# Optimization experiments

Hardware: AMD Instinct MI355X
Metric: run time of the kernel (lower is better)

Reference implementation:

```python
import jax, jax.numpy as jnp
import numpy as np

B, N, C = 8, 1024, 768
H = 12
HD = C // H  # 64
SCALE = HD ** -0.5


def setup_inputs() -> dict:
    key = jax.random.key(0)
    k1, k2, k3, k4 = jax.random.split(key, 4)
    x = jax.random.normal(k1, (B, N, C), dtype=jnp.float32)
    # torch Linear weights are [out, in]; qkv has no bias (qkv_bias=False)
    w_qkv = jax.random.normal(k2, (3 * C, C), dtype=jnp.float32) * (C ** -0.5)
    w_proj = jax.random.normal(k3, (C, C), dtype=jnp.float32) * (C ** -0.5)
    b_proj = jax.random.normal(k4, (C,), dtype=jnp.float32) * 0.01
    return {"x": x, "w_qkv": w_qkv, "w_proj": w_proj, "b_proj": b_proj}


def reference(x, w_qkv, w_proj, b_proj):
    b, n, c = x.shape
    # qkv: [B, N, 3C] -> [3, B, H, N, HD]
    qkv = (x @ w_qkv.T).reshape(b, n, 3, H, c // H).transpose(2, 0, 3, 1, 4)
    q, k, v = qkv[0], qkv[1], qkv[2]
    attn = jnp.einsum('bhqd,bhkd->bhqk', q, k) * SCALE
    attn = jax.nn.softmax(attn, axis=-1)
    out = jnp.einsum('bhqk,bhkd->bhqd', attn, v)          # [B, H, N, HD]
    out = out.transpose(0, 2, 1, 3).reshape(b, n, c)      # [B, N, C]
    out = out @ w_proj.T + b_proj
    return out
```

## Files before the change

kernel.cpp:

```cpp
#include <hip/hip_runtime.h>
#include <hip/hip_bf16.h>
#include <cstdint>

#define TB 8
#define TN 1024
#define TC 768
#define TH 12
#define THD 64
#define TM (TB*TN)
#define TNQKV (3*TC)
#define QSCALE_LOG2E 0.18033688011112042f

typedef __attribute__((ext_vector_type(8))) short s16x8;
typedef __attribute__((ext_vector_type(4))) float f32x4;
typedef __attribute__((ext_vector_type(16))) float f32x16;
typedef __attribute__((ext_vector_type(2))) unsigned int u32x2;

__device__ __forceinline__ unsigned short f2bf(float f) {
    union { float f; unsigned int u; } v; v.f = f;
    unsigned int u = v.u;
    return (unsigned short)((u + 0x7FFFu + ((u >> 16) & 1u)) >> 16);
}

__device__ __forceinline__ float bf2f(unsigned short h) {
    union { float f; unsigned int u; } v; v.u = ((unsigned int)h) << 16;
    return v.f;
}

__device__ __forceinline__ unsigned int cvt_pk_bf16(float lo, float hi) {
    unsigned int r;
    asm("v_cvt_pk_bf16_f32 %0, %1, %2" : "=v"(r) : "v"(lo), "v"(hi));
    return r;
}

__device__ __forceinline__ void gload_lds16(const unsigned short* g, unsigned short* l) {
    __builtin_amdgcn_global_load_lds(
        (const __attribute__((address_space(1))) unsigned int*)g,
        (__attribute__((address_space(3))) unsigned int*)l,
        16, 0, 0);
}

__global__ __launch_bounds__(256) void cvt3_kernel(
    const float* __restrict__ a, unsigned short* __restrict__ oa, int na,
    const float* __restrict__ b, unsigned short* __restrict__ ob, int nb,
    const float* __restrict__ c, unsigned short* __restrict__ oc, int nc)
{
    int i = blockIdx.x * blockDim.x + threadIdx.x;
    const float* src; unsigned short* dst; int idx;
    if (i < na)           { src = a; dst = oa; idx = i; }
    else if (i < na + nb) { src = b; dst = ob; idx = i - na; }
    else if (i < na + nb + nc) { src = c; dst = oc; idx = i - na - nb; }
    else return;
    f32x4 x0 = *(const f32x4*)(src + (size_t)idx * 8);
    f32x4 x1 = *(const f32x4*)(src + (size_t)idx * 8 + 4);
    s16x8 r;
    #pragma unroll
    for (int e = 0; e < 4; e++) r[e] = (short)f2bf(x0[e]);
    #pragma unroll
    for (int e = 0; e < 4; e++) r[4 + e] = (short)f2bf(x1[e]);
    *(s16x8*)(dst + (size_t)idx * 8) = r;
}

template<bool BIAS, bool OBF16, bool VSPLIT>
__global__ __launch_bounds__(256) void gemm_bt(
    const unsigned short* __restrict__ A,
    const unsigned short* __restrict__ Bm,
    void* __restrict__ Cout,
    const float* __restrict__ bias,
    unsigned short* __restrict__ vt,
    int M, int Nn, int K)
{
    __shared__ unsigned short As[128 * 64];
    __shared__ unsigned short Bs[128 * 64];
    const int t = threadIdx.x;
    const int w = t >> 6, l = t & 63;
    const int wm = w >> 1, wn = w & 1;
    const int bm = blockIdx.x, bn = blockIdx.y;
    const int l31 = l & 31, khi = l >> 5;
    const int r7 = l31 & 7;

    f32x16 acc00 = {}, acc01 = {}, acc10 = {}, acc11 = {};

    const unsigned short* Ab = A + (size_t)bm * 128 * K;
    const unsigned short* Bb = Bm + (size_t)bn * 128 * K;

    for (int kt = 0; kt < K; kt += 64) {
        __syncthreads();
        #pragma unroll
        for (int j = 0; j < 4; j++) {
            const int s = j * 256 + t, row = s >> 3, c = s & 7;
            const int g = c ^ (row & 7);
            gload_lds16(Ab + (size_t)row * K + kt + g * 8, As + s * 8);
            gload_lds16(Bb + (size_t)row * K + kt + g * 8, Bs + s * 8);
        }
        __syncthreads();
        #pragma unroll
        for (int ks = 0; ks < 4; ks++) {
            const int ch = ((ks << 1) + khi) ^ r7;
            const unsigned short* Ar = As + (wm * 64 + l31) * 64 + ch * 8;
            const unsigned short* Br = Bs + (wn * 64 + l31) * 64 + ch * 8;
            s16x8 a0 = *(const s16x8*)(Ar);
            s16x8 a1 = *(const s16x8*)(Ar + 32 * 64);
            s16x8 b0 = *(const s16x8*)(Br);
            s16x8 b1 = *(const s16x8*)(Br + 32 * 64);
            acc00 = __builtin_amdgcn_mfma_f32_32x32x16_bf16(a0, b0, acc00, 0, 0, 0);
            acc01 = __builtin_amdgcn_mfma_f32_32x32x16_bf16(a0, b1, acc01, 0, 0, 0);
            acc10 = __builtin_amdgcn_mfma_f32_32x32x16_bf16(a1, b0, acc10, 0, 0, 0);
            acc11 = __builtin_amdgcn_mfma_f32_32x32x16_bf16(a1, b1, acc11, 0, 0, 0);
        }
    }

    const int r0 = bm * 128 + wm * 64;
    const int c0 = bn * 128 + wn * 64;
    f32x16 accs[2][2] = {{acc00, acc01}, {acc10, acc11}};
    if constexpr (VSPLIT) {
        if (bn >= 12) {
            const int bb = (r0 >> 10) * TH;
            #pragma unroll
            for (int X = 0; X < 2; X++)
                #pragma unroll
                for (int Y = 0; Y < 2; Y++) {
                    const int dg = c0 + Y * 32 + l31 - 2 * TC;
                    unsigned short* vp = vt + ((size_t)(bb + (dg >> 6)) << 16)
                                            + (dg & 63) * TN;
                    const int k0 = (r0 & 1023) + X * 32 + 4 * khi;
                    #pragma unroll
                    for (int g = 0; g < 4; g++) {
                        u32x2 r;
                        r[0] = cvt_pk_bf16(accs[X][Y][g * 4], accs[X][Y][g * 4 + 1]);
                        r[1] = cvt_pk_bf16(accs[X][Y][g * 4 + 2], accs[X][Y][g * 4 + 3]);
                        *(u32x2*)(vp + k0 + 8 * g) = r;
                    }
                }
            return;
        }
    }
    if constexpr (OBF16) {
        unsigned short* O = (unsigned short*)Cout;
        #pragma unroll
        for (int X = 0; X < 2; X++)
            #pragma unroll
            for (int Y = 0; Y < 2; Y++) {
                const int cc = c0 + Y * 32 + l31;
                const int rb = r0 + X * 32 + 4 * khi;
                #pragma unroll
                for (int i = 0; i < 16; i++)
                    O[(size_t)(rb + (i & 3) + 8 * (i >> 2)) * Nn + cc] =
                        f2bf(accs[X][Y][i]);
            }
    } else {
        float* O = (float*)Cout;
        #pragma unroll
        for (int X = 0; X < 2; X++)
            #pragma unroll
            for (int Y = 0; Y < 2; Y++) {
                const int cc = c0 + Y * 32 + l31;
                const int rb = r0 + X * 32 + 4 * khi;
                float bv = 0.f;
                if constexpr (BIAS) bv = bias[cc];
                #pragma unroll
                for (int i = 0; i < 16; i++)
                    O[(size_t)(rb + (i & 3) + 8 * (i >> 2)) * Nn + cc] =
                        accs[X][Y][i] + bv;
            }
    }
}

__global__ __launch_bounds__(512) void attn_kernel(
    const unsigned short* __restrict__ qkv,
    const unsigned short* __restrict__ vt,
    unsigned short* __restrict__ out)
{
    const int bid = blockIdx.x;
    const int vid = (bid & 7) * 96 + (bid >> 3);
    const int bh = vid >> 3;
    const int qt = vid & 7;
    const int b = bh / TH, h = bh % TH;
    const int t = threadIdx.x, w = t >> 6, l = t & 63;
    const int lr = l & 15, lh = l >> 4;
    const int qbase = qt * 128 + w * 16;

    __shared__ unsigned short Kbuf[2][64 * 64];
    __shared__ unsigned short Vbuf[2][64 * 64];
    __shared__ unsigned short plds[8][16 * 64];

    const unsigned short* kbase = qkv + (size_t)(b * TN) * TNQKV + TC + h * THD;
    const unsigned short* vtb = vt + (size_t)bh * THD * TN;

    const int srow_lo = (l >> 3);
    const int schunk = (l & 7) ^ srow_lo;
    const int srow = w * 8 + srow_lo;
    const int sdst = w * 512 + l * 8;

    const unsigned short* qptr = qkv + (size_t)(b * TN + qbase + lr) * TNQKV + h * THD;
    s16x8 bq[2];
    #pragma unroll
    for (int cj = 0; cj < 2; cj++) {
        s16x8 raw = *(const s16x8*)(qptr + cj * 32 + lh * 8);
        #pragma unroll
        for (int e = 0; e < 8; e++)
            bq[cj][e] = (short)f2bf(bf2f((unsigned short)raw[e]) * QSCALE_LOG2E);
    }
    s16x8 av1;
    #pragma unroll
    for (int e = 0; e < 8; e++) av1[e] = (short)0x3F80;

    f32x4 o[5] = {};
    unsigned short* pw = plds[w];
    const int lr7 = lr & 7;

    gload_lds16(kbase + (size_t)srow * TNQKV + schunk * 8, &Kbuf[0][sdst]);
    gload_lds16(vtb + (size_t)srow * TN + schunk * 8, &Vbuf[0][sdst]);
    __syncthreads();

    for (int it = 0; it < 16; it++) {
        const int kt = it * 64;
        const int cur = it & 1, nxt = cur ^ 1;
        if (it + 1 < 16) {
            const int ktn = kt + 64;
            gload_lds16(kbase + (size_t)(ktn + srow) * TNQKV + schunk * 8, &Kbuf[nxt][sdst]);
            gload_lds16(vtb + (size_t)srow * TN + ktn + schunk * 8, &Vbuf[nxt][sdst]);
        }
        const unsigned short* Kc = Kbuf[cur];
        const unsigned short* Vc = Vbuf[cur];

        f32x4 s[4];
        __builtin_amdgcn_s_setprio(1);
        #pragma unroll
        for (int kk = 0; kk < 4; kk++) {
            const int r = kk * 16 + lr;
            s16x8 ak0 = *(const s16x8*)(Kc + r * 64 + ((lh ^ lr7) * 8));
            s16x8 ak1 = *(const s16x8*)(Kc + r * 64 + (((4 + lh) ^ lr7) * 8));
            f32x4 z = {0.f, 0.f, 0.f, 0.f};
            z = __builtin_amdgcn_mfma_f32_16x16x32_bf16(ak0, bq[0], z, 0, 0, 0);
            z = __builtin_amdgcn_mfma_f32_16x16x32_bf16(ak1, bq[1], z, 0, 0, 0);
            s[kk] = z;
        }
        __builtin_amdgcn_s_setprio(0);

        #pragma unroll
        for (int kk = 0; kk < 4; kk++)
            #pragma unroll
            for (int i = 0; i < 4; i++)
                s[kk][i] = __builtin_amdgcn_exp2f(s[kk][i]);

        #pragma unroll
        for (int kk = 0; kk < 4; kk++) {
            u32x2 pk;
            pk[0] = cvt_pk_bf16(s[kk][0], s[kk][1]);
            pk[1] = cvt_pk_bf16(s[kk][2], s[kk][3]);
            const int wch = ((kk << 1) + (lh >> 1)) ^ lr7;
            *(u32x2*)(pw + lr * 64 + wch * 8 + (lh & 1) * 4) = pk;
        }
        __builtin_amdgcn_s_setprio(1);
        #pragma unroll
        for (int ktile = 0; ktile < 2; ktile++) {
            const int rch = ((ktile << 2) + lh) ^ lr7;
            s16x8 bp = *(const s16x8*)(pw + lr * 64 + rch * 8);
            #pragma unroll
            for (int nd = 0; nd < 4; nd++) {
                const int d = nd * 16 + lr;
                s16x8 av = *(const s16x8*)(
                    Vc + d * 64 + ((((ktile << 2) + lh) ^ lr7) * 8));
                o[nd] = __builtin_amdgcn_mfma_f32_16x16x32_bf16(av, bp, o[nd], 0, 0, 0);
            }
            o[4] = __builtin_amdgcn_mfma_f32_16x16x32_bf16(av1, bp, o[4], 0, 0, 0);
        }
        __builtin_amdgcn_s_setprio(0);
        __syncthreads();
    }

    float inv = 1.f / o[4][0];
    unsigned short* op = out + (size_t)(b * TN + qbase + lr) * TC + h * THD;
    #pragma unroll
    for (int nd = 0; nd < 4; nd++) {
        u32x2 r;
        r[0] = cvt_pk_bf16(o[nd][0] * inv, o[nd][1] * inv);
        r[1] = cvt_pk_bf16(o[nd][2] * inv, o[nd][3] * inv);
        *(u32x2*)(op + nd * 16 + lh * 4) = r;
    }
}

extern "C" void kernel_launch(void* const* d_in, const int* in_sizes, int n_in,
                              void* d_out, int out_size, void* d_ws, size_t ws_size,
                              hipStream_t stream) {
    const float* x      = (const float*)d_in[0];
    const float* w_qkv  = (const float*)d_in[1];
    const float* w_proj = (const float*)d_in[2];
    const float* b_proj = (const float*)d_in[3];
    float* out = (float*)d_out;

    unsigned short* xb   = (unsigned short*)d_ws;
    unsigned short* wqb  = xb   + (size_t)TM * TC;
    unsigned short* wpb  = wqb  + (size_t)TNQKV * TC;
    unsigned short* qkvb = wpb  + (size_t)TC * TC;
    unsigned short* vtb  = qkvb + (size_t)TM * TNQKV;
    unsigned short* aob  = vtb  + (size_t)TB * TH * THD * TN;

    const int na = TM * TC / 8, nb = TNQKV * TC / 8, nc = TC * TC / 8;
    cvt3_kernel<<<(na + nb + nc + 255) / 256, 256, 0, stream>>>(
        x, xb, na, w_qkv, wqb, nb, w_proj, wpb, nc);

    gemm_bt<false, true, true><<<dim3(TM / 128, TNQKV / 128), 256, 0, stream>>>(
        xb, wqb, (void*)qkvb, nullptr, vtb, TM, TNQKV, TC);

    attn_kernel<<<768, 512, 0, stream>>>(qkvb, vtb, aob);

    gemm_bt<true, false, false><<<dim3(TM / 128, TC / 128), 256, 0, stream>>>(
        aob, wpb, (void*)out, b_proj, nullptr, TM, TC, TC);
}
```

Baseline: 108.8 us.

## Process two 16-row query groups per wave in attention, halving waves per block

The attention block now uses 4 waves of 256 threads instead of 8 waves of 512. Each wave handles 32 query rows as two 16-row groups, so each K and V fragment read from LDS feeds two MFMAs. The K/V tile loads are spread over two iterations per thread to keep the same tile size. This cuts LDS read traffic per unit of work and doubles per-wave MFMA work, at the cost of more registers and fewer waves to hide latency.

```diff
diff --git a/kernel.cpp b/kernel.cpp
--- a/kernel.cpp
+++ b/kernel.cpp
@@ -166,7 +166,7 @@
     }
 }
 
-__global__ __launch_bounds__(512) void attn_kernel(
+__global__ __launch_bounds__(256) void attn_kernel(
     const unsigned short* __restrict__ qkv,
     const unsigned short* __restrict__ vt,
     unsigned short* __restrict__ out)
@@ -178,39 +178,43 @@
     const int b = bh / TH, h = bh % TH;
     const int t = threadIdx.x, w = t >> 6, l = t & 63;
     const int lr = l & 15, lh = l >> 4;
-    const int qbase = qt * 128 + w * 16;
+    const int qbase = qt * 128 + w * 32;
 
     __shared__ unsigned short Kbuf[2][64 * 64];
     __shared__ unsigned short Vbuf[2][64 * 64];
-    __shared__ unsigned short plds[8][16 * 64];
+    __shared__ unsigned short plds[4][32 * 64];
 
     const unsigned short* kbase = qkv + (size_t)(b * TN) * TNQKV + TC + h * THD;
     const unsigned short* vtb = vt + (size_t)bh * THD * TN;
 
-    const int srow_lo = (l >> 3);
-    const int schunk = (l & 7) ^ srow_lo;
-    const int srow = w * 8 + srow_lo;
-    const int sdst = w * 512 + l * 8;
-
-    const unsigned short* qptr = qkv + (size_t)(b * TN + qbase + lr) * TNQKV + h * THD;
-    s16x8 bq[2];
-    #pragma unroll
-    for (int cj = 0; cj < 2; cj++) {
-        s16x8 raw = *(const s16x8*)(qptr + cj * 32 + lh * 8);
-        #pragma unroll
-        for (int e = 0; e < 8; e++)
-            bq[cj][e] = (short)f2bf(bf2f((unsigned short)raw[e]) * QSCALE_LOG2E);
+    s16x8 bq[2][2];
+    #pragma unroll
+    for (int g = 0; g < 2; g++) {
+        const unsigned short* qptr =
+            qkv + (size_t)(b * TN + qbase + g * 16 + lr) * TNQKV + h * THD;
+        #pragma unroll
+        for (int cj = 0; cj < 2; cj++) {
+            s16x8 raw = *(const s16x8*)(qptr + cj * 32 + lh * 8);
+            #pragma unroll
+            for (int e = 0; e < 8; e++)
+                bq[g][cj][e] = (short)f2bf(bf2f((unsigned short)raw[e]) * QSCALE_LOG2E);
+        }
     }
     s16x8 av1;
     #pragma unroll
     for (int e = 0; e < 8; e++) av1[e] = (short)0x3F80;
 
-    f32x4 o[5] = {};
+    f32x4 o[2][5] = {};
     unsigned short* pw = plds[w];
     const int lr7 = lr & 7;
 
-    gload_lds16(kbase + (size_t)srow * TNQKV + schunk * 8, &Kbuf[0][sdst]);
-    gload_lds16(vtb + (size_t)srow * TN + schunk * 8, &Vbuf[0][sdst]);
+    #pragma unroll
+    for (int j = 0; j < 2; j++) {
+        const int s = j * 256 + t, row = s >> 3, c = s & 7;
+        const int g = c ^ (row & 7);
+        gload_lds16(kbase + (size_t)row * TNQKV + g * 8, &Kbuf[0][s * 8]);
+        gload_lds16(vtb + (size_t)row * TN + g * 8, &Vbuf[0][s * 8]);
+    }
     __syncthreads();
 
     for (int it = 0; it < 16; it++) {
@@ -218,66 +222,85 @@
         const int cur = it & 1, nxt = cur ^ 1;
         if (it + 1 < 16) {
             const int ktn = kt + 64;
-            gload_lds16(kbase + (size_t)(ktn + srow) * TNQKV + schunk * 8, &Kbuf[nxt][sdst]);
-            gload_lds16(vtb + (size_t)srow * TN + ktn + schunk * 8, &Vbuf[nxt][sdst]);
+            #pragma unroll
+            for (int j = 0; j < 2; j++) {
+                const int s = j * 256 + t, row = s >> 3, c = s & 7;
+                const int g = c ^ (row & 7);
+                gload_lds16(kbase + (size_t)(ktn + row) * TNQKV + g * 8, &Kbuf[nxt][s * 8]);
+                gload_lds16(vtb + (size_t)row * TN + ktn + g * 8, &Vbuf[nxt][s * 8]);
+            }
         }
         const unsigned short* Kc = Kbuf[cur];
         const unsigned short* Vc = Vbuf[cur];
 
-        f32x4 s[4];
+        f32x4 s[2][4];
         __builtin_amdgcn_s_setprio(1);
         #pragma unroll
         for (int kk = 0; kk < 4; kk++) {
             const int r = kk * 16 + lr;
             s16x8 ak0 = *(const s16x8*)(Kc + r * 64 + ((lh ^ lr7) * 8));
             s16x8 ak1 = *(const s16x8*)(Kc + r * 64 + (((4 + lh) ^ lr7) * 8));
-            f32x4 z = {0.f, 0.f, 0.f, 0.f};
-            z = __builtin_amdgcn_mfma_f32_16x16x32_bf16(ak0, bq[0], z, 0, 0, 0);
-            z = __builtin_amdgcn_mfma_f32_16x16x32_bf16(ak1, bq[1], z, 0, 0, 0);
-            s[kk] = z;
+            #pragma unroll
+            for (int g = 0; g < 2; g++) {
+                f32x4 z = {0.f, 0.f, 0.f, 0.f};
+                z = __builtin_amdgcn_mfma_f32_16x16x32_bf16(ak0, bq[g][0], z, 0, 0, 0);
+                z = __builtin_amdgcn_mfma_f32_16x16x32_bf16(ak1, bq[g][1], z, 0, 0, 0);
+                s[g][kk] = z;
+            }
         }
         __builtin_amdgcn_s_setprio(0);
 
         #pragma unroll
-        for (int kk = 0; kk < 4; kk++)
-            #pragma unroll
-            for (int i = 0; i < 4; i++)
-                s[kk][i] = __builtin_amdgcn_exp2f(s[kk][i]);
-
-        #pragma unroll
-        for (int kk = 0; kk < 4; kk++) {
-            u32x2 pk;
-            pk[0] = cvt_pk_bf16(s[kk][0], s[kk][1]);
-            pk[1] = cvt_pk_bf16(s[kk][2], s[kk][3]);
-            const int wch = ((kk << 1) + (lh >> 1)) ^ lr7;
-            *(u32x2*)(pw + lr * 64 + wch * 8 + (lh & 1) * 4) = pk;
-        }
+        for (int g = 0; g < 2; g++)
+            #pragma unroll
+            for (int kk = 0; kk < 4; kk++)
+                #pragma unroll
+                for (int i = 0; i < 4; i++)
+                    s[g][kk][i] = __builtin_amdgcn_exp2f(s[g][kk][i]);
+
+        #pragma unroll
+        for (int g = 0; g < 2; g++)
+            #pragma unroll
+            for (int kk = 0; kk < 4; kk++) {
+                u32x2 pk;
+                pk[0] = cvt_pk_bf16(s[g][kk][0], s[g][kk][1]);
+                pk[1] = cvt_pk_bf16(s[g][kk][2], s[g][kk][3]);
+                const int wch = ((kk << 1) + (lh >> 1)) ^ lr7;
+                *(u32x2*)(pw + (g * 16 + lr) * 64 + wch * 8 + (lh & 1) * 4) = pk;
+            }
         __builtin_amdgcn_s_setprio(1);
         #pragma unroll
         for (int ktile = 0; ktile < 2; ktile++) {
             const int rch = ((ktile << 2) + lh) ^ lr7;
-            s16x8 bp = *(const s16x8*)(pw + lr * 64 + rch * 8);
+            s16x8 bp0 = *(const s16x8*)(pw + lr * 64 + rch * 8);
+            s16x8 bp1 = *(const s16x8*)(pw + (16 + lr) * 64 + rch * 8);
             #pragma unroll
             for (int nd = 0; nd < 4; nd++) {
                 const int d = nd * 16 + lr;
                 s16x8 av = *(const s16x8*)(
                     Vc + d * 64 + ((((ktile << 2) + lh) ^ lr7) * 8));
-                o[nd] = __builtin_amdgcn_mfma_f32_16x16x32_bf16(av, bp, o[nd], 0, 0, 0);
-            }
-            o[4] = __builtin_amdgcn_mfma_f32_16x16x32_bf16(av1, bp, o[4], 0, 0, 0);
+                o[0][nd] = __builtin_amdgcn_mfma_f32_16x16x32_bf16(av, bp0, o[0][nd], 0, 0, 0);
+                o[1][nd] = __builtin_amdgcn_mfma_f32_16x16x32_bf16(av, bp1, o[1][nd], 0, 0, 0);
+            }
+            o[0][4] = __builtin_amdgcn_mfma_f32_16x16x32_bf16(av1, bp0, o[0][4], 0, 0, 0);
+            o[1][4] = __builtin_amdgcn_mfma_f32_16x16x32_bf16(av1, bp1, o[1][4], 0, 0, 0);
         }
         __builtin_amdgcn_s_setprio(0);
         __syncthreads();
     }
 
-    float inv = 1.f / o[4][0];
-    unsigned short* op = out + (size_t)(b * TN + qbase + lr) * TC + h * THD;
-    #pragma unroll
-    for (int nd = 0; nd < 4; nd++) {
-        u32x2 r;
-        r[0] = cvt_pk_bf16(o[nd][0] * inv, o[nd][1] * inv);
-        r[1] = cvt_pk_bf16(o[nd][2] * inv, o[nd][3] * inv);
-        *(u32x2*)(op + nd * 16 + lh * 4) = r;
+    #pragma unroll
+    for (int g = 0; g < 2; g++) {
+        float inv = 1.f / o[g][4][0];
+        unsigned short* op =
+            out + (size_t)(b * TN + qbase + g * 16 + lr) * TC + h * THD;
+        #pragma unroll
+        for (int nd = 0; nd < 4; nd++) {
+            u32x2 r;
+            r[0] = cvt_pk_bf16(o[g][nd][0] * inv, o[g][nd][1] * inv);
+            r[1] = cvt_pk_bf16(o[g][nd][2] * inv, o[g][nd][3] * inv);
+            *(u32x2*)(op + nd * 16 + lh * 4) = r;
+        }
     }
 }
 
@@ -304,7 +327,7 @@
     gemm_bt<false, true, true><<<dim3(TM / 128, TNQKV / 128), 256, 0, stream>>>(
         xb, wqb, (void*)qkvb, nullptr, vtb, TM, TNQKV, TC);
 
-    attn_kernel<<<768, 512, 0, stream>>>(qkvb, vtb, aob);
+    attn_kernel<<<768, 256, 0, stream>>>(qkvb, vtb, aob);
 
     gemm_bt<true, false, false><<<dim3(TM / 128, TC / 128), 256, 0, stream>>>(
         aob, wpb, (void*)out, b_proj, nullptr, TM, TC, TC);
```

After: 120.9 us. 1.11x slower.
